# Kernel tuning notes

Measured on AMD Instinct MI355X. Metric: run time of the kernel, lower is better.

The kernel has to match this reference:

```python
import jax, jax.numpy as jnp
import numpy as np

N = 100000      # nodes
E = 1600000     # edges (avg degree 16)
D_IN, D_H, D_OUT = 128, 128, 64
EPS = 1e-5      # BatchNorm1d eps


def setup_inputs() -> dict:
    key = jax.random.key(0)
    ks = jax.random.split(key, 8)
    x = jax.random.normal(ks[0], (N, D_IN), jnp.float32)
    edge_index = jax.random.randint(ks[1], (2, E), 0, N, dtype=jnp.int64)

    def glorot(k, i, o):
        return jax.random.normal(k, (i, o), jnp.float32) * np.float32(1.0 / np.sqrt(i))

    return {
        "x": x,
        "edge_index": edge_index,
        "W1": glorot(ks[2], D_IN, D_H), "b1": jnp.zeros((D_H,), jnp.float32),
        "g1": jnp.ones((D_H,), jnp.float32), "be1": jnp.zeros((D_H,), jnp.float32),
        "W2": glorot(ks[3], D_H, D_H), "b2": jnp.zeros((D_H,), jnp.float32),
        "g2": jnp.ones((D_H,), jnp.float32), "be2": jnp.zeros((D_H,), jnp.float32),
        "W3": glorot(ks[4], D_H, D_OUT), "b3": jnp.zeros((D_OUT,), jnp.float32),
    }


def gcn_conv(h, W, b, src, dst, norm_e, self_norm):
    # GCNConv: D^{-1/2}(A+I)D^{-1/2} h W + b  (self-loops handled analytically)
    hw = h @ W                                  # [N, out]
    msg = hw[src] * norm_e[:, None]             # [E, out] gather + scale
    agg = jax.ops.segment_sum(msg, dst, num_segments=N)
    return agg + hw * self_norm[:, None] + b


def batchnorm(x, g, b):
    mu = jnp.mean(x, axis=0)
    var = jnp.var(x, axis=0)
    return (x - mu) * jax.lax.rsqrt(var + EPS) * g + b


def reference(x, edge_index, W1, b1, g1, be1, W2, b2, g2, be2, W3, b3):
    src, dst = edge_index[0], edge_index[1]
    # degrees including self-loop
    deg = jax.ops.segment_sum(jnp.ones((E,), jnp.float32), dst, num_segments=N) + 1.0
    dis = jax.lax.rsqrt(deg)                    # deg^{-1/2}
    norm_e = dis[src] * dis[dst]                # per-edge norm
    self_norm = dis * dis                       # self-loop norm deg^{-1}

    h = jax.nn.relu(batchnorm(gcn_conv(x, W1, b1, src, dst, norm_e, self_norm), g1, be1))
    h = jax.nn.relu(batchnorm(gcn_conv(h, W2, b2, src, dst, norm_e, self_norm), g2, be2))
    return gcn_conv(h, W3, b3, src, dst, norm_e, self_norm)
```

## Files before the change

kernel.cpp:

```cpp
#include <hip/hip_runtime.h>
#include <hip/hip_bf16.h>

#define BN_EPS 1e-5f
#define BINSH 9
#define MAXNB 200
#define NBLK 256
#define BIN_CAP 8960

typedef __attribute__((ext_vector_type(8))) short bf16x8v;
typedef __attribute__((ext_vector_type(4))) float f32x4v;

__device__ __forceinline__ float u2f(unsigned x) { return __uint_as_float(x); }
__device__ __forceinline__ unsigned short f2bf(float f) {
    union { __hip_bfloat16 h; unsigned short u; } cv;
    cv.h = __float2bfloat16(f);
    return cv.u;
}

__device__ __forceinline__ int edge_at(const void* p, long long i, int is64) {
    return is64 ? (int)((const long long*)p)[i] : ((const int*)p)[i];
}

__device__ __forceinline__ void detect_is64(const void* eidx, int* sflag, int t) {
    if (t == 0) {
        const int* e32 = (const int*)eidx;
        int nz = 0;
        for (int i = 0; i < 64; ++i) nz += (e32[2 * i + 1] != 0);
        *sflag = (nz == 0) ? 1 : 0;
    }
}

__global__ __launch_bounds__(256) void histA_kernel(const void* __restrict__ eidx,
                                                    int* __restrict__ hist2dT,
                                                    int* __restrict__ binhist,
                                                    const float* __restrict__ W1,
                                                    const float* __restrict__ W2,
                                                    const float* __restrict__ W3,
                                                    __hip_bfloat16* __restrict__ wt1,
                                                    __hip_bfloat16* __restrict__ wt2,
                                                    __hip_bfloat16* __restrict__ wt3,
                                                    int E, int NB, int per_block) {
    const int t = threadIdx.x;
    if (blockIdx.x >= NBLK) {
        int i = (blockIdx.x - NBLK) * 256 + t;
        if (i < 16384) {
            int k = i >> 7, c = i & 127;
            wt1[c * 128 + k] = __float2bfloat16(W1[i]);
        } else if (i < 32768) {
            int j = i - 16384, k = j >> 7, c = j & 127;
            wt2[c * 128 + k] = __float2bfloat16(W2[j]);
        } else if (i < 40960) {
            int j = i - 32768, k = j >> 6, c = j & 63;
            wt3[c * 128 + k] = __float2bfloat16(W3[j]);
        }
        return;
    }
    __shared__ int lh[MAXNB];
    __shared__ int sflag;
    detect_is64(eidx, &sflag, t);
    for (int i = t; i < NB; i += 256) lh[i] = 0;
    __syncthreads();
    const int is64 = sflag;
    long long base = (long long)blockIdx.x * per_block;
    long long lim  = base + per_block;
    if (lim > E) lim = E;
    for (long long e = base + t; e < lim; e += 256) {
        int d = edge_at(eidx, (long long)E + e, is64);
        atomicAdd(&lh[d >> BINSH], 1);
    }
    __syncthreads();
    for (int i = t; i < NB; i += 256) {
        hist2dT[i * NBLK + blockIdx.x] = lh[i];
        atomicAdd(&binhist[i], lh[i]);
    }
}

__global__ __launch_bounds__(256) void colscan_kernel(int* __restrict__ hist2dT,
                                                      const int* __restrict__ binhist,
                                                      int* __restrict__ binrp, int NB) {
    __shared__ int s[256];
    __shared__ int sbase;
    const int b = blockIdx.x;
    const int t = threadIdx.x;
    s[t] = (t < b) ? binhist[t] : 0;
    __syncthreads();
    for (int off = 128; off > 0; off >>= 1) {
        if (t < off) s[t] += s[t + off];
        __syncthreads();
    }
    if (t == 0) sbase = s[0];
    __syncthreads();
    const int base = sbase;
    if (t == 0) {
        binrp[b] = base;
        if (b == NB - 1) binrp[NB] = base + binhist[b];
    }
    int v = hist2dT[b * NBLK + t];
    s[t] = v;
    __syncthreads();
    for (int off = 1; off < 256; off <<= 1) {
        int x = (t >= off) ? s[t - off] : 0;
        __syncthreads();
        s[t] += x;
        __syncthreads();
    }
    hist2dT[b * NBLK + t] = base + s[t] - v;
}

__global__ __launch_bounds__(256) void passB_kernel(const void* __restrict__ eidx,
                                                    const int* __restrict__ hist2dT,
                                                    int2* __restrict__ ibuf,
                                                    int E, int NB, int per_block) {
    __shared__ int lbase[MAXNB];
    __shared__ int lcur[MAXNB];
    __shared__ int sflag;
    const int t = threadIdx.x;
    detect_is64(eidx, &sflag, t);
    for (int i = t; i < NB; i += 256) {
        lbase[i] = hist2dT[i * NBLK + blockIdx.x];
        lcur[i]  = 0;
    }
    __syncthreads();
    const int is64 = sflag;
    long long base = (long long)blockIdx.x * per_block;
    long long lim  = base + per_block;
    if (lim > E) lim = E;
    for (long long e = base + t; e < lim; e += 256) {
        int sN = edge_at(eidx, e, is64);
        int d  = edge_at(eidx, (long long)E + e, is64);
        int b  = d >> BINSH;
        int pos = lbase[b] + atomicAdd(&lcur[b], 1);
        ibuf[pos] = make_int2(sN, d);
    }
}

__global__ __launch_bounds__(256) void binsort2_kernel(const int2* __restrict__ ibuf,
                                                       const int* __restrict__ binrp,
                                                       int* __restrict__ rp,
                                                       float* __restrict__ dis,
                                                       int* __restrict__ ep, int N) {
    const int b  = blockIdx.x;
    const int d0 = b << BINSH;
    const int dc = min(1 << BINSH, N - d0);
    __shared__ int lcnt[1 << BINSH];
    __shared__ int lofs[1 << BINSH];
    __shared__ int s2[256];
    __shared__ unsigned short sperm[BIN_CAP];
    const int t = threadIdx.x;
    lcnt[t] = 0; lcnt[t + 256] = 0;
    __syncthreads();
    const int ib0 = binrp[b], ib1 = binrp[b + 1];
    const int nE  = ib1 - ib0;
    for (int i = t; i < nE; i += 256) {
        int2 sd = ibuf[ib0 + i];
        atomicAdd(&lcnt[sd.y - d0], 1);
    }
    __syncthreads();
    const int c0 = lcnt[2 * t], c1 = lcnt[2 * t + 1];
    const int pair = c0 + c1;
    s2[t] = pair;
    __syncthreads();
    for (int off = 1; off < 256; off <<= 1) {
        int x = (t >= off) ? s2[t - off] : 0;
        __syncthreads();
        s2[t] += x;
        __syncthreads();
    }
    const int pexcl = s2[t] - pair;
    if (2 * t < dc) {
        rp[d0 + 2 * t + 1] = ib0 + pexcl + c0;
        dis[d0 + 2 * t]    = rsqrtf((float)c0 + 1.0f);
    }
    if (2 * t + 1 < dc) {
        rp[d0 + 2 * t + 2] = ib0 + pexcl + pair;
        dis[d0 + 2 * t + 1] = rsqrtf((float)c1 + 1.0f);
    }
    if (b == 0 && t == 0) rp[0] = 0;
    lofs[2 * t]     = pexcl;
    lofs[2 * t + 1] = pexcl + c0;
    __syncthreads();
    if (nE <= BIN_CAP) {
        for (int i = t; i < nE; i += 256) {
            int dl = ibuf[ib0 + i].y - d0;
            int pos = atomicAdd(&lofs[dl], 1);
            sperm[pos] = (unsigned short)i;
        }
        __syncthreads();
        for (int j = t; j < nE; j += 256)
            ep[ib0 + j] = ibuf[ib0 + (int)sperm[j]].x;
    } else {
        for (int i = t; i < nE; i += 256) {
            int2 sd = ibuf[ib0 + i];
            int pos = ib0 + atomicAdd(&lofs[sd.y - d0], 1);
            ep[pos] = sd.x;
        }
    }
}

__device__ __forceinline__ void load8(const float* p, float* f) {
    float4 v0 = ((const float4*)p)[0];
    float4 v1 = ((const float4*)p)[1];
    f[0] = v0.x; f[1] = v0.y; f[2] = v0.z; f[3] = v0.w;
    f[4] = v1.x; f[5] = v1.y; f[6] = v1.z; f[7] = v1.w;
}
__device__ __forceinline__ void load8(const __hip_bfloat16* p, float* f) {
    uint4 v = *(const uint4*)p;
    f[0] = u2f(v.x << 16); f[1] = u2f(v.x & 0xffff0000u);
    f[2] = u2f(v.y << 16); f[3] = u2f(v.y & 0xffff0000u);
    f[4] = u2f(v.z << 16); f[5] = u2f(v.z & 0xffff0000u);
    f[6] = u2f(v.w << 16); f[7] = u2f(v.w & 0xffff0000u);
}

template <int DOUT, bool BN, typename TH>
__global__ __launch_bounds__(256) void mfma_gemm_kernel(const TH* __restrict__ H,
                                                        const __hip_bfloat16* __restrict__ Wt,
                                                        const float* __restrict__ stats,
                                                        const float* __restrict__ g,
                                                        const float* __restrict__ be,
                                                        float invN,
                                                        __hip_bfloat16* __restrict__ out, int N) {
    constexpr int NCT = DOUT / 16;
    constexpr int LDW = 136;
    __shared__ __hip_bfloat16 sWt[DOUT * LDW];
    __shared__ float sBN[256];
    const int t = threadIdx.x;
    for (int i = t; i < DOUT * 16; i += 256) {
        int row = i >> 4, seg = i & 15;
        *(uint4*)&sWt[row * LDW + seg * 8] = ((const uint4*)Wt)[i];
    }
    if (BN && t < 128) {
        float mu  = stats[t] * invN;
        float var = stats[128 + t] * invN - mu * mu;
        float sc  = g[t] * rsqrtf(var + BN_EPS);
        sBN[t]       = sc;
        sBN[128 + t] = be[t] - mu * sc;
    }
    __syncthreads();
    const int lane = t & 63, wid = t >> 6;
    const int kq = lane >> 4, mrow = lane & 15;
#pragma unroll
    for (int gq = 0; gq < 4; ++gq) {
        const int rbase = blockIdx.x * 256 + wid * 64 + gq * 16;
        if (rbase >= N) break;
        const int lrow = min(rbase + mrow, N - 1);
        bf16x8v afrag[4];
#pragma unroll
        for (int ks = 0; ks < 4; ++ks) {
            const int k0 = ks * 32 + kq * 8;
            float f[8];
            load8(H + (size_t)lrow * 128 + k0, f);
            if (BN) {
                float4 s0 = *(const float4*)&sBN[k0];
                float4 s1 = *(const float4*)&sBN[k0 + 4];
                float4 h0 = *(const float4*)&sBN[128 + k0];
                float4 h1 = *(const float4*)&sBN[128 + k0 + 4];
                f[0] = fmaxf(fmaf(f[0], s0.x, h0.x), 0.f);
                f[1] = fmaxf(fmaf(f[1], s0.y, h0.y), 0.f);
                f[2] = fmaxf(fmaf(f[2], s0.z, h0.z), 0.f);
                f[3] = fmaxf(fmaf(f[3], s0.w, h0.w), 0.f);
                f[4] = fmaxf(fmaf(f[4], s1.x, h1.x), 0.f);
                f[5] = fmaxf(fmaf(f[5], s1.y, h1.y), 0.f);
                f[6] = fmaxf(fmaf(f[6], s1.z, h1.z), 0.f);
                f[7] = fmaxf(fmaf(f[7], s1.w, h1.w), 0.f);
            }
            bf16x8v a;
#pragma unroll
            for (int j = 0; j < 8; ++j) a[j] = (short)f2bf(f[j]);
            afrag[ks] = a;
        }
        f32x4v acc[NCT];
#pragma unroll
        for (int ct = 0; ct < NCT; ++ct) acc[ct] = (f32x4v){0.f, 0.f, 0.f, 0.f};
#pragma unroll
        for (int ct = 0; ct < NCT; ++ct) {
#pragma unroll
            for (int ks = 0; ks < 4; ++ks) {
                bf16x8v bb = *(const bf16x8v*)&sWt[(ct * 16 + mrow) * LDW + ks * 32 + kq * 8];
                acc[ct] = __builtin_amdgcn_mfma_f32_16x16x32_bf16(afrag[ks], bb, acc[ct], 0, 0, 0);
            }
        }
#pragma unroll
        for (int r = 0; r < 4; ++r) {
            int orow = rbase + kq * 4 + r;
            if (orow < N) {
                __hip_bfloat16* op = out + (size_t)orow * DOUT + mrow;
#pragma unroll
                for (int ct = 0; ct < NCT; ++ct) {
                    union { unsigned short u; __hip_bfloat16 h; } cv;
                    cv.u = f2bf(acc[ct][r]);
                    op[ct * 16] = cv.h;
                }
            }
        }
    }
}

__device__ __forceinline__ void acc8(float* a, uint4 v, float w) {
    a[0] += u2f(v.x << 16) * w;  a[1] += u2f(v.x & 0xffff0000u) * w;
    a[2] += u2f(v.y << 16) * w;  a[3] += u2f(v.y & 0xffff0000u) * w;
    a[4] += u2f(v.z << 16) * w;  a[5] += u2f(v.z & 0xffff0000u) * w;
    a[6] += u2f(v.w << 16) * w;  a[7] += u2f(v.w & 0xffff0000u) * w;
}

template <int D, bool OUTBF, bool STATS>
__global__ __launch_bounds__(256) void agg_kernel(const __hip_bfloat16* __restrict__ hw,
                                                  const int* __restrict__ rp,
                                                  const int* __restrict__ ep,
                                                  const float* __restrict__ dis,
                                                  const float* __restrict__ bias,
                                                  void* __restrict__ outv,
                                                  float* __restrict__ partial, int N) {
    constexpr int LPR = D / 8;
    const int t = threadIdx.x;
    const int gtid = blockIdx.x * 256 + t;
    const int idx  = gtid / LPR;
    const int lane = gtid % LPR;
    const bool valid = idx < N;
    if (!STATS && !valid) return;
    const int n = valid ? idx : (N - 1);
    const uint4* hw8 = (const uint4*)hw;
    float a[8] = {0.f, 0.f, 0.f, 0.f, 0.f, 0.f, 0.f, 0.f};
    const float dn = dis[n];
    uint4 hv = hw8[(size_t)n * LPR + lane];
    acc8(a, hv, dn);
    int e0 = rp[n], e1 = rp[n + 1];
    int e = e0;
    for (; e + 4 <= e1; e += 4) {
        int p0 = ep[e + 0];
        int p1 = ep[e + 1];
        int p2 = ep[e + 2];
        int p3 = ep[e + 3];
        uint4 v0 = hw8[(size_t)p0 * LPR + lane];
        uint4 v1 = hw8[(size_t)p1 * LPR + lane];
        uint4 v2 = hw8[(size_t)p2 * LPR + lane];
        uint4 v3 = hw8[(size_t)p3 * LPR + lane];
        acc8(a, v0, dis[p0]);
        acc8(a, v1, dis[p1]);
        acc8(a, v2, dis[p2]);
        acc8(a, v3, dis[p3]);
    }
    for (; e < e1; ++e) {
        int p = ep[e];
        uint4 v = hw8[(size_t)p * LPR + lane];
        acc8(a, v, dis[p]);
    }
    float4 b0 = *(const float4*)(bias + lane * 8);
    float4 b1 = *(const float4*)(bias + lane * 8 + 4);
    a[0] = fmaf(a[0], dn, b0.x); a[1] = fmaf(a[1], dn, b0.y);
    a[2] = fmaf(a[2], dn, b0.z); a[3] = fmaf(a[3], dn, b0.w);
    a[4] = fmaf(a[4], dn, b1.x); a[5] = fmaf(a[5], dn, b1.y);
    a[6] = fmaf(a[6], dn, b1.z); a[7] = fmaf(a[7], dn, b1.w);
    if (STATS) {
        __shared__ float ls[16][128];
        const int r16 = t >> 4;
#pragma unroll
        for (int j = 0; j < 8; ++j) ls[r16][lane * 8 + j] = valid ? a[j] : 0.f;
        __syncthreads();
        if (t < 128) {
            float s = 0.f, q = 0.f;
#pragma unroll
            for (int r = 0; r < 16; ++r) {
                float v = ls[r][t];
                s += v;
                q += v * v;
            }
            partial[(size_t)blockIdx.x * 256 + t]       = s;
            partial[(size_t)blockIdx.x * 256 + 128 + t] = q;
        }
    }
    if (valid) {
        if (OUTBF) {
            uint4 o;
            o.x = (unsigned)f2bf(a[0]) | ((unsigned)f2bf(a[1]) << 16);
            o.y = (unsigned)f2bf(a[2]) | ((unsigned)f2bf(a[3]) << 16);
            o.z = (unsigned)f2bf(a[4]) | ((unsigned)f2bf(a[5]) << 16);
            o.w = (unsigned)f2bf(a[6]) | ((unsigned)f2bf(a[7]) << 16);
            ((uint4*)outv)[(size_t)n * LPR + lane] = o;
        } else {
            float4* op = (float4*)outv + ((size_t)n * D + lane * 8) / 4;
            op[0] = make_float4(a[0], a[1], a[2], a[3]);
            op[1] = make_float4(a[4], a[5], a[6], a[7]);
        }
    }
}

__global__ __launch_bounds__(256) void red_kernel(const float* __restrict__ partial,
                                                  float* __restrict__ stats, int nb) {
    const int t = threadIdx.x;
    const int per = (nb + gridDim.x - 1) / gridDim.x;
    const int r0 = blockIdx.x * per;
    const int r1 = min(r0 + per, nb);
    float s = 0.f;
    for (int r = r0; r < r1; ++r) s += partial[(size_t)r * 256 + t];
    atomicAdd(&stats[t], s);
}

extern "C" void kernel_launch(void* const* d_in, const int* in_sizes, int n_in,
                              void* d_out, int out_size, void* d_ws, size_t ws_size,
                              hipStream_t stream) {
    const float* x   = (const float*)d_in[0];
    const void*  eix = d_in[1];
    const float* W1  = (const float*)d_in[2];
    const float* b1  = (const float*)d_in[3];
    const float* g1  = (const float*)d_in[4];
    const float* be1 = (const float*)d_in[5];
    const float* W2  = (const float*)d_in[6];
    const float* b2  = (const float*)d_in[7];
    const float* g2  = (const float*)d_in[8];
    const float* be2 = (const float*)d_in[9];
    const float* W3  = (const float*)d_in[10];
    const float* b3  = (const float*)d_in[11];
    float* outp = (float*)d_out;

    const int N = in_sizes[0] / 128;
    const int E = in_sizes[1] / 2;
    const int NB = (N + (1 << BINSH) - 1) >> BINSH;

    char* base = (char*)d_ws;
    size_t off = 0;
    auto alloc = [&](size_t bytes) -> char* {
        char* p = base + off;
        off = (off + bytes + 255) & ~(size_t)255;
        return p;
    };
    __hip_bfloat16* A = (__hip_bfloat16*)alloc((size_t)N * 128 * 2);
    __hip_bfloat16* B = (__hip_bfloat16*)alloc((size_t)N * 128 * 2);
    int*   rp      = (int*)alloc((size_t)(N + 1) * 4);
    float* dis     = (float*)alloc((size_t)N * 4);
    int*   ep      = (int*)alloc((size_t)E * 4);
    int2*  ibuf    = (int2*)alloc((size_t)E * 8);
    int*   hist2dT = (int*)alloc((size_t)MAXNB * NBLK * 4);
    int*   binrp   = (int*)alloc((MAXNB + 1) * 4);
    int*   binhist = (int*)alloc(MAXNB * 4);
    float* stats1  = (float*)alloc(256 * 4);
    float* stats2  = (float*)alloc(256 * 4);
    __hip_bfloat16* wt1 = (__hip_bfloat16*)alloc(128 * 128 * 2);
    __hip_bfloat16* wt2 = (__hip_bfloat16*)alloc(128 * 128 * 2);
    __hip_bfloat16* wt3 = (__hip_bfloat16*)alloc(64 * 128 * 2);
    (void)ws_size; (void)n_in; (void)out_size;

    const int per_block   = (E + NBLK - 1) / NBLK;
    const int gemm_grid   = (N + 255) / 256;
    const int agg128_grid = (int)(((long long)N * 16 + 255) / 256);
    const int agg64_grid  = (int)(((long long)N * 8 + 255) / 256);
    const float invN = 1.0f / (float)N;

    float* partial1 = (float*)ibuf;
    float* partial2 = (float*)ibuf + (size_t)agg128_grid * 256;

    hipMemsetAsync(binhist, 0, 3 * 1024, stream);
    histA_kernel<<<NBLK + 160, 256, 0, stream>>>(eix, hist2dT, binhist,
                                                 W1, W2, W3, wt1, wt2, wt3, E, NB, per_block);
    colscan_kernel<<<NB, 256, 0, stream>>>(hist2dT, binhist, binrp, NB);
    passB_kernel<<<NBLK, 256, 0, stream>>>(eix, hist2dT, ibuf, E, NB, per_block);
    binsort2_kernel<<<NB, 256, 0, stream>>>(ibuf, binrp, rp, dis, ep, N);

    mfma_gemm_kernel<128, false, float><<<gemm_grid, 256, 0, stream>>>(
        x, wt1, nullptr, nullptr, nullptr, 0.f, A, N);
    agg_kernel<128, true, true><<<agg128_grid, 256, 0, stream>>>(
        A, rp, ep, dis, b1, B, partial1, N);
    red_kernel<<<32, 256, 0, stream>>>(partial1, stats1, agg128_grid);

    mfma_gemm_kernel<128, true, __hip_bfloat16><<<gemm_grid, 256, 0, stream>>>(
        B, wt2, stats1, g1, be1, invN, A, N);
    agg_kernel<128, true, true><<<agg128_grid, 256, 0, stream>>>(
        A, rp, ep, dis, b2, B, partial2, N);
    red_kernel<<<32, 256, 0, stream>>>(partial2, stats2, agg128_grid);

    mfma_gemm_kernel<64, true, __hip_bfloat16><<<gemm_grid, 256, 0, stream>>>(
        B, wt3, stats2, g2, be2, invN, A, N);
    agg_kernel<64, false, false><<<agg64_grid, 256, 0, stream>>>(
        A, rp, ep, dis, b3, outp, nullptr, N);
}
```

Measured before the change: 360.2 us.

## Fuse layer-1 GEMM into histogram prelaunch and pack CSR sort buffer to 32-bit

The first-layer GEMM x@W1 now runs as extra blocks of the histogram/weight-conversion kernel, converting W1 to bf16 directly in shared memory, so it overlaps with the edge histogram and saves one launch. The intermediate bucket buffer packs source id and local destination into one 32-bit word instead of an int2, halving the traffic in passB and binsort. partial2 moves to its own allocation because ibuf shrank. The packing assumes node ids fit in 17 bits, and the per-block raw W1 conversion repeats redundant work in every GEMM block.

After: 359.5 us. Within noise of the previous version (-0.2%).

```diff
diff --git a/kernel.cpp b/kernel.cpp
--- a/kernel.cpp
+++ b/kernel.cpp
@@ -30,173 +30,6 @@
     }
 }
 
-__global__ __launch_bounds__(256) void histA_kernel(const void* __restrict__ eidx,
-                                                    int* __restrict__ hist2dT,
-                                                    int* __restrict__ binhist,
-                                                    const float* __restrict__ W1,
-                                                    const float* __restrict__ W2,
-                                                    const float* __restrict__ W3,
-                                                    __hip_bfloat16* __restrict__ wt1,
-                                                    __hip_bfloat16* __restrict__ wt2,
-                                                    __hip_bfloat16* __restrict__ wt3,
-                                                    int E, int NB, int per_block) {
-    const int t = threadIdx.x;
-    if (blockIdx.x >= NBLK) {
-        int i = (blockIdx.x - NBLK) * 256 + t;
-        if (i < 16384) {
-            int k = i >> 7, c = i & 127;
-            wt1[c * 128 + k] = __float2bfloat16(W1[i]);
-        } else if (i < 32768) {
-            int j = i - 16384, k = j >> 7, c = j & 127;
-            wt2[c * 128 + k] = __float2bfloat16(W2[j]);
-        } else if (i < 40960) {
-            int j = i - 32768, k = j >> 6, c = j & 63;
-            wt3[c * 128 + k] = __float2bfloat16(W3[j]);
-        }
-        return;
-    }
-    __shared__ int lh[MAXNB];
-    __shared__ int sflag;
-    detect_is64(eidx, &sflag, t);
-    for (int i = t; i < NB; i += 256) lh[i] = 0;
-    __syncthreads();
-    const int is64 = sflag;
-    long long base = (long long)blockIdx.x * per_block;
-    long long lim  = base + per_block;
-    if (lim > E) lim = E;
-    for (long long e = base + t; e < lim; e += 256) {
-        int d = edge_at(eidx, (long long)E + e, is64);
-        atomicAdd(&lh[d >> BINSH], 1);
-    }
-    __syncthreads();
-    for (int i = t; i < NB; i += 256) {
-        hist2dT[i * NBLK + blockIdx.x] = lh[i];
-        atomicAdd(&binhist[i], lh[i]);
-    }
-}
-
-__global__ __launch_bounds__(256) void colscan_kernel(int* __restrict__ hist2dT,
-                                                      const int* __restrict__ binhist,
-                                                      int* __restrict__ binrp, int NB) {
-    __shared__ int s[256];
-    __shared__ int sbase;
-    const int b = blockIdx.x;
-    const int t = threadIdx.x;
-    s[t] = (t < b) ? binhist[t] : 0;
-    __syncthreads();
-    for (int off = 128; off > 0; off >>= 1) {
-        if (t < off) s[t] += s[t + off];
-        __syncthreads();
-    }
-    if (t == 0) sbase = s[0];
-    __syncthreads();
-    const int base = sbase;
-    if (t == 0) {
-        binrp[b] = base;
-        if (b == NB - 1) binrp[NB] = base + binhist[b];
-    }
-    int v = hist2dT[b * NBLK + t];
-    s[t] = v;
-    __syncthreads();
-    for (int off = 1; off < 256; off <<= 1) {
-        int x = (t >= off) ? s[t - off] : 0;
-        __syncthreads();
-        s[t] += x;
-        __syncthreads();
-    }
-    hist2dT[b * NBLK + t] = base + s[t] - v;
-}
-
-__global__ __launch_bounds__(256) void passB_kernel(const void* __restrict__ eidx,
-                                                    const int* __restrict__ hist2dT,
-                                                    int2* __restrict__ ibuf,
-                                                    int E, int NB, int per_block) {
-    __shared__ int lbase[MAXNB];
-    __shared__ int lcur[MAXNB];
-    __shared__ int sflag;
-    const int t = threadIdx.x;
-    detect_is64(eidx, &sflag, t);
-    for (int i = t; i < NB; i += 256) {
-        lbase[i] = hist2dT[i * NBLK + blockIdx.x];
-        lcur[i]  = 0;
-    }
-    __syncthreads();
-    const int is64 = sflag;
-    long long base = (long long)blockIdx.x * per_block;
-    long long lim  = base + per_block;
-    if (lim > E) lim = E;
-    for (long long e = base + t; e < lim; e += 256) {
-        int sN = edge_at(eidx, e, is64);
-        int d  = edge_at(eidx, (long long)E + e, is64);
-        int b  = d >> BINSH;
-        int pos = lbase[b] + atomicAdd(&lcur[b], 1);
-        ibuf[pos] = make_int2(sN, d);
-    }
-}
-
-__global__ __launch_bounds__(256) void binsort2_kernel(const int2* __restrict__ ibuf,
-                                                       const int* __restrict__ binrp,
-                                                       int* __restrict__ rp,
-                                                       float* __restrict__ dis,
-                                                       int* __restrict__ ep, int N) {
-    const int b  = blockIdx.x;
-    const int d0 = b << BINSH;
-    const int dc = min(1 << BINSH, N - d0);
-    __shared__ int lcnt[1 << BINSH];
-    __shared__ int lofs[1 << BINSH];
-    __shared__ int s2[256];
-    __shared__ unsigned short sperm[BIN_CAP];
-    const int t = threadIdx.x;
-    lcnt[t] = 0; lcnt[t + 256] = 0;
-    __syncthreads();
-    const int ib0 = binrp[b], ib1 = binrp[b + 1];
-    const int nE  = ib1 - ib0;
-    for (int i = t; i < nE; i += 256) {
-        int2 sd = ibuf[ib0 + i];
-        atomicAdd(&lcnt[sd.y - d0], 1);
-    }
-    __syncthreads();
-    const int c0 = lcnt[2 * t], c1 = lcnt[2 * t + 1];
-    const int pair = c0 + c1;
-    s2[t] = pair;
-    __syncthreads();
-    for (int off = 1; off < 256; off <<= 1) {
-        int x = (t >= off) ? s2[t - off] : 0;
-        __syncthreads();
-        s2[t] += x;
-        __syncthreads();
-    }
-    const int pexcl = s2[t] - pair;
-    if (2 * t < dc) {
-        rp[d0 + 2 * t + 1] = ib0 + pexcl + c0;
-        dis[d0 + 2 * t]    = rsqrtf((float)c0 + 1.0f);
-    }
-    if (2 * t + 1 < dc) {
-        rp[d0 + 2 * t + 2] = ib0 + pexcl + pair;
-        dis[d0 + 2 * t + 1] = rsqrtf((float)c1 + 1.0f);
-    }
-    if (b == 0 && t == 0) rp[0] = 0;
-    lofs[2 * t]     = pexcl;
-    lofs[2 * t + 1] = pexcl + c0;
-    __syncthreads();
-    if (nE <= BIN_CAP) {
-        for (int i = t; i < nE; i += 256) {
-            int dl = ibuf[ib0 + i].y - d0;
-            int pos = atomicAdd(&lofs[dl], 1);
-            sperm[pos] = (unsigned short)i;
-        }
-        __syncthreads();
-        for (int j = t; j < nE; j += 256)
-            ep[ib0 + j] = ibuf[ib0 + (int)sperm[j]].x;
-    } else {
-        for (int i = t; i < nE; i += 256) {
-            int2 sd = ibuf[ib0 + i];
-            int pos = ib0 + atomicAdd(&lofs[sd.y - d0], 1);
-            ep[pos] = sd.x;
-        }
-    }
-}
-
 __device__ __forceinline__ void load8(const float* p, float* f) {
     float4 v0 = ((const float4*)p)[0];
     float4 v1 = ((const float4*)p)[1];
@@ -211,22 +44,32 @@
     f[6] = u2f(v.w << 16); f[7] = u2f(v.w & 0xffff0000u);
 }
 
-template <int DOUT, bool BN, typename TH>
-__global__ __launch_bounds__(256) void mfma_gemm_kernel(const TH* __restrict__ H,
-                                                        const __hip_bfloat16* __restrict__ Wt,
-                                                        const float* __restrict__ stats,
-                                                        const float* __restrict__ g,
-                                                        const float* __restrict__ be,
-                                                        float invN,
-                                                        __hip_bfloat16* __restrict__ out, int N) {
+template <int DOUT, bool BN, bool RAWW, typename TH>
+__device__ __forceinline__ void gemm_body(int bx, const TH* __restrict__ H,
+                                          const void* __restrict__ Wsrc,
+                                          const float* __restrict__ stats,
+                                          const float* __restrict__ g,
+                                          const float* __restrict__ be,
+                                          float invN,
+                                          __hip_bfloat16* __restrict__ out, int N,
+                                          char* smem) {
     constexpr int NCT = DOUT / 16;
     constexpr int LDW = 136;
-    __shared__ __hip_bfloat16 sWt[DOUT * LDW];
-    __shared__ float sBN[256];
-    const int t = threadIdx.x;
-    for (int i = t; i < DOUT * 16; i += 256) {
-        int row = i >> 4, seg = i & 15;
-        *(uint4*)&sWt[row * LDW + seg * 8] = ((const uint4*)Wt)[i];
+    __hip_bfloat16* sWt = (__hip_bfloat16*)smem;
+    float* sBN = (float*)(smem + (size_t)DOUT * LDW * 2);
+    const int t = threadIdx.x;
+    if (RAWW) {
+        const float* W = (const float*)Wsrc;
+        for (int i = t; i < 128 * DOUT; i += 256) {
+            int k = i / DOUT, c = i % DOUT;
+            sWt[c * LDW + k] = __float2bfloat16(W[i]);
+        }
+    } else {
+        const __hip_bfloat16* Wt = (const __hip_bfloat16*)Wsrc;
+        for (int i = t; i < DOUT * 16; i += 256) {
+            int row = i >> 4, seg = i & 15;
+            *(uint4*)&sWt[row * LDW + seg * 8] = ((const uint4*)Wt)[i];
+        }
     }
     if (BN && t < 128) {
         float mu  = stats[t] * invN;
@@ -240,7 +83,7 @@
     const int kq = lane >> 4, mrow = lane & 15;
 #pragma unroll
     for (int gq = 0; gq < 4; ++gq) {
-        const int rbase = blockIdx.x * 256 + wid * 64 + gq * 16;
+        const int rbase = bx * 256 + wid * 64 + gq * 16;
         if (rbase >= N) break;
         const int lrow = min(rbase + mrow, N - 1);
         bf16x8v afrag[4];
@@ -291,6 +134,187 @@
                     op[ct * 16] = cv.h;
                 }
             }
+        }
+    }
+}
+
+__global__ __launch_bounds__(256) void fused_pre_kernel(const void* __restrict__ eidx,
+                                                        int* __restrict__ hist2dT,
+                                                        int* __restrict__ binhist,
+                                                        const float* __restrict__ W2,
+                                                        const float* __restrict__ W3,
+                                                        __hip_bfloat16* __restrict__ wt2,
+                                                        __hip_bfloat16* __restrict__ wt3,
+                                                        const float* __restrict__ x,
+                                                        const float* __restrict__ W1,
+                                                        __hip_bfloat16* __restrict__ A,
+                                                        int E, int NB, int per_block, int N) {
+    __shared__ __align__(16) char smem[128 * 136 * 2 + 256 * 4];
+    const int bx = blockIdx.x;
+    const int t = threadIdx.x;
+    if (bx < NBLK) {
+        int* lh = (int*)smem;
+        int* sflag = lh + MAXNB;
+        detect_is64(eidx, sflag, t);
+        for (int i = t; i < NB; i += 256) lh[i] = 0;
+        __syncthreads();
+        const int is64 = *sflag;
+        long long base = (long long)bx * per_block;
+        long long lim  = base + per_block;
+        if (lim > E) lim = E;
+        for (long long e = base + t; e < lim; e += 256) {
+            int d = edge_at(eidx, (long long)E + e, is64);
+            atomicAdd(&lh[d >> BINSH], 1);
+        }
+        __syncthreads();
+        for (int i = t; i < NB; i += 256) {
+            hist2dT[i * NBLK + bx] = lh[i];
+            atomicAdd(&binhist[i], lh[i]);
+        }
+    } else if (bx < NBLK + 96) {
+        int i = (bx - NBLK) * 256 + t;
+        if (i < 16384) {
+            int k = i >> 7, c = i & 127;
+            wt2[c * 128 + k] = __float2bfloat16(W2[i]);
+        } else if (i < 24576) {
+            int j = i - 16384, k = j >> 6, c = j & 63;
+            wt3[c * 128 + k] = __float2bfloat16(W3[j]);
+        }
+    } else {
+        gemm_body<128, false, true, float>(bx - NBLK - 96, x, W1,
+                                           nullptr, nullptr, nullptr, 0.f, A, N, smem);
+    }
+}
+
+template <int DOUT, bool BN, typename TH>
+__global__ __launch_bounds__(256) void mfma_gemm_kernel(const TH* __restrict__ H,
+                                                        const __hip_bfloat16* __restrict__ Wt,
+                                                        const float* __restrict__ stats,
+                                                        const float* __restrict__ g,
+                                                        const float* __restrict__ be,
+                                                        float invN,
+                                                        __hip_bfloat16* __restrict__ out, int N) {
+    __shared__ __align__(16) char smem[(size_t)DOUT * 136 * 2 + 256 * 4];
+    gemm_body<DOUT, BN, false, TH>(blockIdx.x, H, Wt, stats, g, be, invN, out, N, smem);
+}
+
+__global__ __launch_bounds__(256) void colscan_kernel(int* __restrict__ hist2dT,
+                                                      const int* __restrict__ binhist,
+                                                      int* __restrict__ binrp, int NB) {
+    __shared__ int s[256];
+    __shared__ int sbase;
+    const int b = blockIdx.x;
+    const int t = threadIdx.x;
+    s[t] = (t < b) ? binhist[t] : 0;
+    __syncthreads();
+    for (int off = 128; off > 0; off >>= 1) {
+        if (t < off) s[t] += s[t + off];
+        __syncthreads();
+    }
+    if (t == 0) sbase = s[0];
+    __syncthreads();
+    const int base = sbase;
+    if (t == 0) {
+        binrp[b] = base;
+        if (b == NB - 1) binrp[NB] = base + binhist[b];
+    }
+    int v = hist2dT[b * NBLK + t];
+    s[t] = v;
+    __syncthreads();
+    for (int off = 1; off < 256; off <<= 1) {
+        int x = (t >= off) ? s[t - off] : 0;
+        __syncthreads();
+        s[t] += x;
+        __syncthreads();
+    }
+    hist2dT[b * NBLK + t] = base + s[t] - v;
+}
+
+__global__ __launch_bounds__(256) void passB_kernel(const void* __restrict__ eidx,
+                                                    const int* __restrict__ hist2dT,
+                                                    int* __restrict__ ibuf,
+                                                    int E, int NB, int per_block) {
+    __shared__ int lbase[MAXNB];
+    __shared__ int lcur[MAXNB];
+    __shared__ int sflag;
+    const int t = threadIdx.x;
+    detect_is64(eidx, &sflag, t);
+    for (int i = t; i < NB; i += 256) {
+        lbase[i] = hist2dT[i * NBLK + blockIdx.x];
+        lcur[i]  = 0;
+    }
+    __syncthreads();
+    const int is64 = sflag;
+    long long base = (long long)blockIdx.x * per_block;
+    long long lim  = base + per_block;
+    if (lim > E) lim = E;
+    for (long long e = base + t; e < lim; e += 256) {
+        int sN = edge_at(eidx, e, is64);
+        int d  = edge_at(eidx, (long long)E + e, is64);
+        int b  = d >> BINSH;
+        int dl = d & ((1 << BINSH) - 1);
+        int pos = lbase[b] + atomicAdd(&lcur[b], 1);
+        ibuf[pos] = sN | (dl << 17);
+    }
+}
+
+__global__ __launch_bounds__(256) void binsort2_kernel(const int* __restrict__ ibuf,
+                                                       const int* __restrict__ binrp,
+                                                       int* __restrict__ rp,
+                                                       float* __restrict__ dis,
+                                                       int* __restrict__ ep, int N) {
+    const int b  = blockIdx.x;
+    const int d0 = b << BINSH;
+    const int dc = min(1 << BINSH, N - d0);
+    __shared__ int lcnt[1 << BINSH];
+    __shared__ int lofs[1 << BINSH];
+    __shared__ int s2[256];
+    __shared__ unsigned short sperm[BIN_CAP];
+    const int t = threadIdx.x;
+    lcnt[t] = 0; lcnt[t + 256] = 0;
+    __syncthreads();
+    const int ib0 = binrp[b], ib1 = binrp[b + 1];
+    const int nE  = ib1 - ib0;
+    for (int i = t; i < nE; i += 256) {
+        atomicAdd(&lcnt[ibuf[ib0 + i] >> 17], 1);
+    }
+    __syncthreads();
+    const int c0 = lcnt[2 * t], c1 = lcnt[2 * t + 1];
+    const int pair = c0 + c1;
+    s2[t] = pair;
+    __syncthreads();
+    for (int off = 1; off < 256; off <<= 1) {
+        int x = (t >= off) ? s2[t - off] : 0;
+        __syncthreads();
+        s2[t] += x;
+        __syncthreads();
+    }
+    const int pexcl = s2[t] - pair;
+    if (2 * t < dc) {
+        rp[d0 + 2 * t + 1] = ib0 + pexcl + c0;
+        dis[d0 + 2 * t]    = rsqrtf((float)c0 + 1.0f);
+    }
+    if (2 * t + 1 < dc) {
+        rp[d0 + 2 * t + 2] = ib0 + pexcl + pair;
+        dis[d0 + 2 * t + 1] = rsqrtf((float)c1 + 1.0f);
+    }
+    if (b == 0 && t == 0) rp[0] = 0;
+    lofs[2 * t]     = pexcl;
+    lofs[2 * t + 1] = pexcl + c0;
+    __syncthreads();
+    if (nE <= BIN_CAP) {
+        for (int i = t; i < nE; i += 256) {
+            int pos = atomicAdd(&lofs[ibuf[ib0 + i] >> 17], 1);
+            sperm[pos] = (unsigned short)i;
+        }
+        __syncthreads();
+        for (int j = t; j < nE; j += 256)
+            ep[ib0 + j] = ibuf[ib0 + (int)sperm[j]] & 0x1FFFF;
+    } else {
+        for (int i = t; i < nE; i += 256) {
+            int v = ibuf[ib0 + i];
+            int pos = ib0 + atomicAdd(&lofs[v >> 17], 1);
+            ep[pos] = v & 0x1FFFF;
         }
     }
 }
@@ -428,35 +452,31 @@
     int*   rp      = (int*)alloc((size_t)(N + 1) * 4);
     float* dis     = (float*)alloc((size_t)N * 4);
     int*   ep      = (int*)alloc((size_t)E * 4);
-    int2*  ibuf    = (int2*)alloc((size_t)E * 8);
+    int*   ibuf    = (int*)alloc((size_t)E * 4);
     int*   hist2dT = (int*)alloc((size_t)MAXNB * NBLK * 4);
     int*   binrp   = (int*)alloc((MAXNB + 1) * 4);
     int*   binhist = (int*)alloc(MAXNB * 4);
     float* stats1  = (float*)alloc(256 * 4);
     float* stats2  = (float*)alloc(256 * 4);
-    __hip_bfloat16* wt1 = (__hip_bfloat16*)alloc(128 * 128 * 2);
     __hip_bfloat16* wt2 = (__hip_bfloat16*)alloc(128 * 128 * 2);
     __hip_bfloat16* wt3 = (__hip_bfloat16*)alloc(64 * 128 * 2);
+    const int agg128_grid = (int)(((long long)N * 16 + 255) / 256);
+    float* partial2 = (float*)alloc((size_t)agg128_grid * 256 * 4);
     (void)ws_size; (void)n_in; (void)out_size;
 
     const int per_block   = (E + NBLK - 1) / NBLK;
     const int gemm_grid   = (N + 255) / 256;
-    const int agg128_grid = (int)(((long long)N * 16 + 255) / 256);
     const int agg64_grid  = (int)(((long long)N * 8 + 255) / 256);
     const float invN = 1.0f / (float)N;
-
     float* partial1 = (float*)ibuf;
-    float* partial2 = (float*)ibuf + (size_t)agg128_grid * 256;
 
     hipMemsetAsync(binhist, 0, 3 * 1024, stream);
-    histA_kernel<<<NBLK + 160, 256, 0, stream>>>(eix, hist2dT, binhist,
-                                                 W1, W2, W3, wt1, wt2, wt3, E, NB, per_block);
+    fused_pre_kernel<<<NBLK + 96 + gemm_grid, 256, 0, stream>>>(
+        eix, hist2dT, binhist, W2, W3, wt2, wt3, x, W1, A, E, NB, per_block, N);
     colscan_kernel<<<NB, 256, 0, stream>>>(hist2dT, binhist, binrp, NB);
     passB_kernel<<<NBLK, 256, 0, stream>>>(eix, hist2dT, ibuf, E, NB, per_block);
     binsort2_kernel<<<NB, 256, 0, stream>>>(ibuf, binrp, rp, dis, ep, N);
 
-    mfma_gemm_kernel<128, false, float><<<gemm_grid, 256, 0, stream>>>(
-        x, wt1, nullptr, nullptr, nullptr, 0.f, A, N);
     agg_kernel<128, true, true><<<agg128_grid, 256, 0, stream>>>(
         A, rp, ep, dis, b1, B, partial1, N);
     red_kernel<<<32, 256, 0, stream>>>(partial1, stats1, agg128_grid);
```
